# Kernel optimization log

Hardware: AMD Instinct MI355X
Metric: run time of the kernel (lower is better)

Reference implementation:

```python
import jax, jax.numpy as jnp
import numpy as np

B, D, H = 65536, 128, 64


def setup_inputs() -> dict:
    key = jax.random.key(0)
    ks = jax.random.split(key, 20)
    p = lambda k, shp, fan: jax.random.normal(k, shp, jnp.float32) * (1.0 / np.sqrt(fan))
    return {
        "l": jax.random.normal(ks[0], (B, D), jnp.float32),
        "a": jax.random.normal(ks[1], (B, D), jnp.float32),
        "v": jax.random.normal(ks[2], (B, D), jnp.float32),
        "att_w": p(ks[3], (D, 1), D), "att_b": jnp.zeros((1,), jnp.float32),
        "gf_w1": p(ks[4], (2 * D, H), 2 * D), "gf_b1": jnp.zeros((H,), jnp.float32),
        "gf_w2": p(ks[5], (H, D), H), "gf_b2": jnp.zeros((D,), jnp.float32),
        "gf2_w1": p(ks[6], (2 * D, H), 2 * D), "gf2_b1": jnp.zeros((H,), jnp.float32),
        "gf2_w2": p(ks[7], (H, D), H), "gf2_b2": jnp.zeros((D,), jnp.float32),
        "ll_w1": p(ks[8], (3 * D, H), 3 * D), "ll_b1": jnp.zeros((H,), jnp.float32),
        "ll_w2": p(ks[9], (H, H), H), "ll_b2": jnp.zeros((H,), jnp.float32),
        "ll_w3": p(ks[10], (H, D), H), "ll_b3": jnp.zeros((D,), jnp.float32),
    }


def reference(l, a, v, att_w, att_b, gf_w1, gf_b1, gf_w2, gf_b2,
              gf2_w1, gf2_b1, gf2_w2, gf2_b2,
              ll_w1, ll_b1, ll_w2, ll_b2, ll_w3, ll_b3):
    def gf(x, y):  # graph_fusion on cat([x,y],1): Linear->LeakyReLU(0.2)->Linear->Tanh
        h = jnp.concatenate([x, y], 1) @ gf_w1 + gf_b1
        h = jax.nn.leaky_relu(h, 0.2)
        return jnp.tanh(h @ gf_w2 + gf_b2)

    def gf2(x, y):
        h = jnp.concatenate([x, y], 1) @ gf2_w1 + gf2_b1
        h = jax.nn.leaky_relu(h, 0.2)
        return jnp.tanh(h @ gf2_w2 + gf2_b2)

    dot = lambda x, y: jnp.sum(x * y, axis=1)  # batched [B,1,d]@[B,d,1] -> [B]

    sa = jnp.tanh(a @ att_w + att_b)  # [B,1]
    sv = jnp.tanh(v @ att_w + att_b)
    sl = jnp.tanh(l @ att_w + att_b)

    unimodal = (sa * a + sv * v + sl * l) / 3.0  # [B,D]
    sa1, sv1, sl1 = sa[:, 0], sv[:, 0], sl[:, 0]

    # modalities are overwritten by softmax in the original
    a = jax.nn.softmax(a, axis=1)
    v = jax.nn.softmax(v, axis=1)
    l = jax.nn.softmax(l, axis=1)

    sav = (sa1 + sv1) / (dot(a, v) + 0.5)
    sal = (sa1 + sl1) / (dot(a, l) + 0.5)
    svl = (sl1 + sv1) / (dot(v, l) + 0.5)
    normalize = jax.nn.softmax(jnp.stack([sav, sal, svl], axis=1), axis=1)  # [B,3]

    gav, gal, gvl = gf(a, v), gf(a, l), gf(v, l)  # reused (torch computes twice)
    a_v = jnp.tanh(normalize[:, 0:1] * gav)
    a_l = jnp.tanh(normalize[:, 1:2] * gal)
    v_l = jnp.tanh(normalize[:, 2:3] * gvl)
    bimodal = a_v + a_l + v_l

    a_v2 = jax.nn.softmax(gav, axis=1)
    a_l2 = jax.nn.softmax(gal, axis=1)
    v_l2 = jax.nn.softmax(gvl, axis=1)

    savvl = (sav + svl) / (dot(a_v2, v_l2) + 0.5)
    saavl = (sav + sal) / (dot(a_v2, a_l2) + 0.5)
    savll = (sal + svl) / (dot(a_l2, v_l2) + 0.5)
    savl = (sav + sl1) / (dot(a_v2, l) + 0.5)
    salv = (sal + sv1) / (dot(a_l2, v) + 0.5)
    svla = (sa1 + svl) / (dot(v_l2, a) + 0.5)
    n2 = jax.nn.softmax(jnp.stack([savvl, saavl, savll, savl, salv, svla], axis=1), axis=1)

    trimodal = (jnp.tanh(n2[:, 0:1] * gf2(a_v, v_l))
                + jnp.tanh(n2[:, 1:2] * gf2(a_v, a_l))
                + jnp.tanh(n2[:, 2:3] * gf2(v_l, a_l))
                + jnp.tanh(n2[:, 3:4] * gf2(a_v, l))
                + jnp.tanh(n2[:, 4:5] * gf2(a_l, v))
                + jnp.tanh(n2[:, 5:6] * gf2(v_l, a)))

    fusion = jnp.concatenate([unimodal, bimodal, trimodal], axis=1)  # [B,3D]
    h = jnp.tanh(fusion @ ll_w1 + ll_b1)
    h = jnp.tanh(h @ ll_w2 + ll_b2)
    return jnp.tanh(h @ ll_w3 + ll_b3)
```

## Files before the change

### kernel.cpp

```cpp
#include <hip/hip_runtime.h>

typedef short bfrag __attribute__((ext_vector_type(8)));
typedef float facc  __attribute__((ext_vector_type(4)));
typedef unsigned short u16;
typedef unsigned int   u32;

#define LOG2E 1.4426950408889634f
#define MFMA(A,B,C) __builtin_amdgcn_mfma_f32_16x16x32_bf16((A),(B),(C),0,0,0)

#define AS_E 0
#define VS_E 2176
#define LS_E 4352
#define AV_E 6528
#define AL_E 8704
#define VL_E 10880
#define FUS_E 13056
#define HH_E 19328
#define SCR_B 52480
#define SM_BYTES 53504

__device__ __forceinline__ float ex2(float x){ return __builtin_amdgcn_exp2f(x); }
__device__ __forceinline__ float rcpf_(float x){ return __builtin_amdgcn_rcpf(x); }
__device__ __forceinline__ float ftanh(float x){ return 1.0f - 2.0f*rcpf_(ex2(x*(2.0f*LOG2E)) + 1.0f); }
__device__ __forceinline__ u16 f2b(float x){ return (u16)((__float_as_uint(x) + 0x8000u)>>16); }
__device__ __forceinline__ float b2f(u16 b){ return __uint_as_float(((u32)b)<<16); }
__device__ __forceinline__ u32 pk2(float x0, float x1){
  return __builtin_amdgcn_perm(__float_as_uint(x1)+0x8000u, __float_as_uint(x0)+0x8000u, 0x07060302u);
}
__device__ __forceinline__ float rsum16(float v){
  v += __shfl_xor(v,1); v += __shfl_xor(v,2); v += __shfl_xor(v,4); v += __shfl_xor(v,8); return v;
}
__device__ __forceinline__ float rmax16(float v){
  v = fmaxf(v,__shfl_xor(v,1)); v = fmaxf(v,__shfl_xor(v,2));
  v = fmaxf(v,__shfl_xor(v,4)); v = fmaxf(v,__shfl_xor(v,8)); return v;
}
__device__ __forceinline__ void st4b(u16* p, float x0,float x1,float x2,float x3){
  *(uint2*)p = make_uint2(pk2(x0,x1), pk2(x2,x3));
}

__global__ void prep_weights(const float* __restrict__ gf_w1, const float* __restrict__ gf_w2,
                             const float* __restrict__ gf2_w1, const float* __restrict__ gf2_w2,
                             const float* __restrict__ ll_w1, const float* __restrict__ ll_w2,
                             const float* __restrict__ ll_w3, u16* __restrict__ blob)
{
  u32 i = blockIdx.x*256u + threadIdx.x;
  if (i >= 86016u) return;
  u32 off, K, N; const float* src;
  if      (i < 16384u){ off=0u;     K=256u; N=64u;  src=gf_w1; }
  else if (i < 24576u){ off=16384u; K=64u;  N=128u; src=gf_w2; }
  else if (i < 40960u){ off=24576u; K=256u; N=64u;  src=gf2_w1; }
  else if (i < 49152u){ off=40960u; K=64u;  N=128u; src=gf2_w2; }
  else if (i < 73728u){ off=49152u; K=384u; N=64u;  src=ll_w1; }
  else if (i < 77824u){ off=73728u; K=64u;  N=64u;  src=ll_w2; }
  else               { off=77824u; K=64u;  N=128u; src=ll_w3; }
  u32 li = i - off, n = li / K, k = li - n*K;
  blob[i] = f2b(src[k*N + n]);
}

__global__ __launch_bounds__(256,3) void fused_graph(
    const float* __restrict__ Lg, const float* __restrict__ Ag, const float* __restrict__ Vg,
    const float* __restrict__ att_w, const float* __restrict__ att_b,
    const float* __restrict__ gf_b1, const float* __restrict__ gf_b2,
    const float* __restrict__ gf2_b1, const float* __restrict__ gf2_b2,
    const float* __restrict__ ll_b1, const float* __restrict__ ll_b2, const float* __restrict__ ll_b3,
    const u16* __restrict__ wb, float* __restrict__ out)
{
  __shared__ alignas(16) char sm[SM_BYTES];
  u16* smu = (u16*)sm;
  float* scr = (float*)(sm + SCR_B);

  const int tid = threadIdx.x;
  const int lane = tid & 63;
  const int w = tid >> 6;
  const int m = lane & 15;
  const int q = lane >> 4;
  const int er = tid >> 4;
  const int ep = tid & 15;
  const int row0 = blockIdx.x << 4;

  const int gb = (row0 + er)*128 + ep*4;
  facc A0 = *(const facc*)(Ag+gb), A1 = *(const facc*)(Ag+gb+64);
  facc V0 = *(const facc*)(Vg+gb), V1 = *(const facc*)(Vg+gb+64);
  facc L0 = *(const facc*)(Lg+gb), L1 = *(const facc*)(Lg+gb+64);
  facc W0 = *(const facc*)(att_w+ep*4), W1 = *(const facc*)(att_w+ep*4+64);
  float ab = att_b[0];
  float pa=0.f,pv=0.f,pl=0.f;
  #pragma unroll
  for (int i=0;i<4;i++){ pa += A0[i]*W0[i]+A1[i]*W1[i]; pv += V0[i]*W0[i]+V1[i]*W1[i]; pl += L0[i]*W0[i]+L1[i]*W1[i]; }
  float sa = ftanh(rsum16(pa)+ab), sv = ftanh(rsum16(pv)+ab), sl = ftanh(rsum16(pl)+ab);
  {
    u16* fu = smu + FUS_E + er*392 + ep*4;
    const float th = 1.0f/3.0f;
    st4b(fu,    (sa*A0[0]+sv*V0[0]+sl*L0[0])*th, (sa*A0[1]+sv*V0[1]+sl*L0[1])*th,
                (sa*A0[2]+sv*V0[2]+sl*L0[2])*th, (sa*A0[3]+sv*V0[3]+sl*L0[3])*th);
    st4b(fu+64, (sa*A1[0]+sv*V1[0]+sl*L1[0])*th, (sa*A1[1]+sv*V1[1]+sl*L1[1])*th,
                (sa*A1[2]+sv*V1[2]+sl*L1[2])*th, (sa*A1[3]+sv*V1[3]+sl*L1[3])*th);
  }
  #define SMAX(X0,X1,OFFE) { \
    float mx=-3.0e38f; \
    _Pragma("unroll") for (int i=0;i<4;i++){ mx=fmaxf(mx,fmaxf(X0[i],X1[i])); } \
    mx = rmax16(mx); float s_=0.f; \
    _Pragma("unroll") for (int i=0;i<4;i++){ X0[i]=ex2((X0[i]-mx)*LOG2E); X1[i]=ex2((X1[i]-mx)*LOG2E); s_+=X0[i]+X1[i]; } \
    s_ = rsum16(s_); float rs_ = rcpf_(s_); \
    _Pragma("unroll") for (int i=0;i<4;i++){ X0[i]*=rs_; X1[i]*=rs_; } \
    u16* dp_ = smu + (OFFE) + er*136 + ep*4; \
    st4b(dp_, X0[0],X0[1],X0[2],X0[3]); st4b(dp_+64, X1[0],X1[1],X1[2],X1[3]); }
  SMAX(A0,A1,AS_E)
  SMAX(V0,V1,VS_E)
  SMAX(L0,L1,LS_E)
  float dav=0.f,dal=0.f,dvl=0.f;
  #pragma unroll
  for (int i=0;i<4;i++){ dav += A0[i]*V0[i]+A1[i]*V1[i]; dal += A0[i]*L0[i]+A1[i]*L1[i]; dvl += V0[i]*L0[i]+V1[i]*L1[i]; }
  dav = rsum16(dav); dal = rsum16(dal); dvl = rsum16(dvl);
  float sav = (sa+sv)*rcpf_(dav+0.5f);
  float sal = (sa+sl)*rcpf_(dal+0.5f);
  float svl = (sl+sv)*rcpf_(dvl+0.5f);
  if (ep==0){
    float mx = fmaxf(sav,fmaxf(sal,svl));
    float e0 = ex2((sav-mx)*LOG2E), e1 = ex2((sal-mx)*LOG2E), e2 = ex2((svl-mx)*LOG2E);
    float rs = rcpf_(e0+e1+e2);
    scr[er*16+0]=e0*rs; scr[er*16+1]=e1*rs; scr[er*16+2]=e2*rs;
  }
  __syncthreads();

  const u16* g1t = wb;
  const u16* g2t = wb + 16384;
  bfrag B1[8];
  #pragma unroll
  for (int s=0;s<8;s++) B1[s] = *(const bfrag*)(g1t + (w*16+m)*256 + s*32 + q*8);
  bfrag B2[2][2];
  #pragma unroll
  for (int t=0;t<2;t++){
    #pragma unroll
    for (int s=0;s<2;s++) B2[t][s] = *(const bfrag*)(g2t + ((w+4*t)*16+m)*64 + s*32 + q*8);
  }
  facc acc0={0,0,0,0}, acc1={0,0,0,0}, acc2={0,0,0,0};
  #pragma unroll
  for (int s=0;s<8;s++){
    int k = s*32 + q*8, ko = k & 127; bool hi = (k >= 128);
    const u16* p0 = smu + (hi? VS_E:AS_E) + m*136 + ko;
    const u16* p1 = smu + (hi? LS_E:AS_E) + m*136 + ko;
    const u16* p2 = smu + (hi? LS_E:VS_E) + m*136 + ko;
    acc0 = MFMA(*(const bfrag*)p0, B1[s], acc0);
    acc1 = MFMA(*(const bfrag*)p1, B1[s], acc1);
    acc2 = MFMA(*(const bfrag*)p2, B1[s], acc2);
  }
  {
    float b1v = gf_b1[w*16+m];
    #pragma unroll
    for (int r=0;r<4;r++){
      int rr = q*4+r;
      float h0 = acc0[r]+b1v; h0 = fmaxf(h0, 0.2f*h0);
      float h1 = acc1[r]+b1v; h1 = fmaxf(h1, 0.2f*h1);
      float h2 = acc2[r]+b1v; h2 = fmaxf(h2, 0.2f*h2);
      smu[HH_E + 0*1152 + rr*72 + w*16+m] = f2b(h0);
      smu[HH_E + 1*1152 + rr*72 + w*16+m] = f2b(h1);
      smu[HH_E + 2*1152 + rr*72 + w*16+m] = f2b(h2);
    }
  }
  __syncthreads();
  facc c2[3][2] = {{{0,0,0,0},{0,0,0,0}},{{0,0,0,0},{0,0,0,0}},{{0,0,0,0},{0,0,0,0}}};
  #pragma unroll
  for (int s=0;s<2;s++){
    int k = s*32 + q*8;
    #pragma unroll
    for (int p3=0;p3<3;p3++){
      bfrag Af = *(const bfrag*)(smu + HH_E + p3*1152 + m*72 + k);
      c2[p3][0] = MFMA(Af, B2[0][s], c2[p3][0]);
      c2[p3][1] = MFMA(Af, B2[1][s], c2[p3][1]);
    }
  }
  __syncthreads();
  {
    float b2v0 = gf_b2[w*16+m], b2v1 = gf_b2[(w+4)*16+m];
    float bim[2][4] = {{0,0,0,0},{0,0,0,0}};
    float nv[4][3];
    #pragma unroll
    for (int r=0;r<4;r++){ int rr=q*4+r; nv[r][0]=scr[rr*16+0]; nv[r][1]=scr[rr*16+1]; nv[r][2]=scr[rr*16+2]; }
    #pragma unroll
    for (int p3=0;p3<3;p3++){
      #pragma unroll
      for (int t=0;t<2;t++){
        float bb = t? b2v1 : b2v0;
        int cc = (w+4*t)*16+m;
        #pragma unroll
        for (int r=0;r<4;r++){
          int rr=q*4+r;
          float g = ftanh(c2[p3][t][r] + bb);
          smu[HH_E + p3*2048 + rr*128 + cc] = f2b(g);
          float tt = ftanh(nv[r][p3]*g);
          smu[AV_E + p3*2176 + rr*136 + cc] = f2b(tt);
          bim[t][r] += tt;
        }
      }
    }
    #pragma unroll
    for (int t=0;t<2;t++){
      #pragma unroll
      for (int r=0;r<4;r++)
        smu[FUS_E + (q*4+r)*392 + 128 + (w+4*t)*16+m] = f2b(bim[t][r]);
    }
  }
  __syncthreads();

  float E0[8], E1[8], E2[8];
  #define GSTAT(EA, G3) { \
    const u16* gp_ = smu + HH_E + (G3)*2048 + er*128 + ep*4; \
    float x_[8]; \
    _Pragma("unroll") for (int i=0;i<4;i++){ x_[i]=b2f(gp_[i]); x_[4+i]=b2f(gp_[64+i]); } \
    float mx_=-3.0e38f; \
    _Pragma("unroll") for (int j=0;j<8;j++) mx_=fmaxf(mx_,x_[j]); \
    mx_ = rmax16(mx_); float s_=0.f; \
    _Pragma("unroll") for (int j=0;j<8;j++){ x_[j]=ex2((x_[j]-mx_)*LOG2E); s_+=x_[j]; } \
    s_ = rsum16(s_); float rs_=rcpf_(s_); \
    _Pragma("unroll") for (int j=0;j<8;j++) EA[j]=x_[j]*rs_; }
  GSTAT(E0,0)
  GSTAT(E1,1)
  GSTAT(E2,2)
  float d01=0.f,d02=0.f,d12=0.f,d0l=0.f,d1v=0.f,d2a=0.f;
  #pragma unroll
  for (int i=0;i<4;i++){
    d01 += E0[i]*E1[i] + E0[4+i]*E1[4+i];
    d02 += E0[i]*E2[i] + E0[4+i]*E2[4+i];
    d12 += E1[i]*E2[i] + E1[4+i]*E2[4+i];
    d0l += E0[i]*L0[i] + E0[4+i]*L1[i];
    d1v += E1[i]*V0[i] + E1[4+i]*V1[i];
    d2a += E2[i]*A0[i] + E2[4+i]*A1[i];
  }
  d01=rsum16(d01); d02=rsum16(d02); d12=rsum16(d12);
  d0l=rsum16(d0l); d1v=rsum16(d1v); d2a=rsum16(d2a);
  if (ep==0){
    float x0 = (sav+svl)*rcpf_(d02+0.5f);
    float x1 = (sav+sal)*rcpf_(d01+0.5f);
    float x2 = (sal+svl)*rcpf_(d12+0.5f);
    float x3 = (sav+sl )*rcpf_(d0l+0.5f);
    float x4 = (sal+sv )*rcpf_(d1v+0.5f);
    float x5 = (sa +svl)*rcpf_(d2a+0.5f);
    float mx = fmaxf(fmaxf(fmaxf(x0,x1),fmaxf(x2,x3)),fmaxf(x4,x5));
    float e0=ex2((x0-mx)*LOG2E), e1=ex2((x1-mx)*LOG2E), e2=ex2((x2-mx)*LOG2E);
    float e3=ex2((x3-mx)*LOG2E), e4=ex2((x4-mx)*LOG2E), e5=ex2((x5-mx)*LOG2E);
    float rs = rcpf_(e0+e1+e2+e3+e4+e5);
    scr[er*16+ 9]=e0*rs; scr[er*16+10]=e1*rs; scr[er*16+11]=e2*rs;
    scr[er*16+12]=e3*rs; scr[er*16+13]=e4*rs; scr[er*16+14]=e5*rs;
  }
  __syncthreads();

  const u16* h1t = wb + 24576;
  const u16* h2t = wb + 40960;
  bfrag C1[8];
  #pragma unroll
  for (int s=0;s<8;s++) C1[s] = *(const bfrag*)(h1t + (w*16+m)*256 + s*32 + q*8);
  bfrag C2[2][2];
  #pragma unroll
  for (int t=0;t<2;t++){
    #pragma unroll
    for (int s=0;s<2;s++) C2[t][s] = *(const bfrag*)(h2t + ((w+4*t)*16+m)*64 + s*32 + q*8);
  }
  const int S0[6] = {AV_E, AV_E, VL_E, AV_E, AL_E, VL_E};
  const int S1[6] = {VL_E, AL_E, AL_E, LS_E, VS_E, AS_E};
  facc cc1[6];
  #pragma unroll
  for (int pr=0;pr<6;pr++){ facc z = {0,0,0,0}; cc1[pr] = z; }
  #pragma unroll
  for (int s=0;s<8;s++){
    int k = s*32+q*8, ko = k&127; bool hi = (k>=128);
    #pragma unroll
    for (int pr=0;pr<6;pr++){
      const u16* sp = smu + (hi? S1[pr]:S0[pr]) + m*136 + ko;
      cc1[pr] = MFMA(*(const bfrag*)sp, C1[s], cc1[pr]);
    }
  }
  {
    float b1v = gf2_b1[w*16+m];
    #pragma unroll
    for (int pr=0;pr<6;pr++){
      #pragma unroll
      for (int r=0;r<4;r++){
        float h = cc1[pr][r]+b1v; h = fmaxf(h,0.2f*h);
        smu[HH_E + pr*1152 + (q*4+r)*72 + w*16+m] = f2b(h);
      }
    }
  }
  __syncthreads();
  facc cc2[6][2];
  #pragma unroll
  for (int pr=0;pr<6;pr++){ facc z = {0,0,0,0}; cc2[pr][0]=z; cc2[pr][1]=z; }
  #pragma unroll
  for (int s=0;s<2;s++){
    int k=s*32+q*8;
    #pragma unroll
    for (int pr=0;pr<6;pr++){
      bfrag Af = *(const bfrag*)(smu + HH_E + pr*1152 + m*72 + k);
      cc2[pr][0] = MFMA(Af, C2[0][s], cc2[pr][0]);
      cc2[pr][1] = MFMA(Af, C2[1][s], cc2[pr][1]);
    }
  }
  {
    float b2v0 = gf2_b2[w*16+m], b2v1 = gf2_b2[(w+4)*16+m];
    float tri[2][4] = {{0,0,0,0},{0,0,0,0}};
    float n2v[4][6];
    #pragma unroll
    for (int r=0;r<4;r++){
      #pragma unroll
      for (int j=0;j<6;j++) n2v[r][j] = scr[(q*4+r)*16+9+j];
    }
    #pragma unroll
    for (int pr=0;pr<6;pr++){
      #pragma unroll
      for (int t=0;t<2;t++){
        float bb = t? b2v1 : b2v0;
        #pragma unroll
        for (int r=0;r<4;r++){
          float g = ftanh(cc2[pr][t][r] + bb);
          tri[t][r] += ftanh(n2v[r][pr]*g);
        }
      }
    }
    #pragma unroll
    for (int t=0;t<2;t++){
      #pragma unroll
      for (int r=0;r<4;r++)
        smu[FUS_E + (q*4+r)*392 + 256 + (w+4*t)*16+m] = f2b(tri[t][r]);
    }
  }
  __syncthreads();

  const u16* lw1 = wb + 49152;
  const u16* lw2 = wb + 73728;
  const u16* lw3 = wb + 77824;
  {
    facc c = {0,0,0,0};
    #pragma unroll
    for (int s=0;s<12;s++){
      bfrag Bf = *(const bfrag*)(lw1 + (w*16+m)*384 + s*32 + q*8);
      bfrag Af = *(const bfrag*)(smu + FUS_E + m*392 + s*32 + q*8);
      c = MFMA(Af, Bf, c);
    }
    float b = ll_b1[w*16+m];
    #pragma unroll
    for (int r=0;r<4;r++) smu[HH_E + (q*4+r)*72 + w*16+m] = f2b(ftanh(c[r]+b));
  }
  __syncthreads();
  {
    facc c = {0,0,0,0};
    #pragma unroll
    for (int s=0;s<2;s++){
      bfrag Bf = *(const bfrag*)(lw2 + (w*16+m)*64 + s*32 + q*8);
      bfrag Af = *(const bfrag*)(smu + HH_E + m*72 + s*32 + q*8);
      c = MFMA(Af, Bf, c);
    }
    float b = ll_b2[w*16+m];
    #pragma unroll
    for (int r=0;r<4;r++) smu[HH_E + 1152 + (q*4+r)*72 + w*16+m] = f2b(ftanh(c[r]+b));
  }
  __syncthreads();
  {
    facc c0={0,0,0,0}, c1={0,0,0,0};
    #pragma unroll
    for (int s=0;s<2;s++){
      bfrag Af  = *(const bfrag*)(smu + HH_E + 1152 + m*72 + s*32 + q*8);
      bfrag Bf0 = *(const bfrag*)(lw3 + (w*16+m)*64 + s*32 + q*8);
      bfrag Bf1 = *(const bfrag*)(lw3 + ((w+4)*16+m)*64 + s*32 + q*8);
      c0 = MFMA(Af, Bf0, c0);
      c1 = MFMA(Af, Bf1, c1);
    }
    float b0 = ll_b3[w*16+m], b1 = ll_b3[(w+4)*16+m];
    #pragma unroll
    for (int r=0;r<4;r++){
      out[(row0+q*4+r)*128 + w*16+m]        = ftanh(c0[r]+b0);
      out[(row0+q*4+r)*128 + (w+4)*16+m]    = ftanh(c1[r]+b1);
    }
  }
}

extern "C" void kernel_launch(void* const* d_in, const int* in_sizes, int n_in,
                              void* d_out, int out_size, void* d_ws, size_t ws_size,
                              hipStream_t stream)
{
  const float* l      = (const float*)d_in[0];
  const float* a      = (const float*)d_in[1];
  const float* v      = (const float*)d_in[2];
  const float* att_w  = (const float*)d_in[3];
  const float* att_b  = (const float*)d_in[4];
  const float* gf_w1  = (const float*)d_in[5];
  const float* gf_b1  = (const float*)d_in[6];
  const float* gf_w2  = (const float*)d_in[7];
  const float* gf_b2  = (const float*)d_in[8];
  const float* gf2_w1 = (const float*)d_in[9];
  const float* gf2_b1 = (const float*)d_in[10];
  const float* gf2_w2 = (const float*)d_in[11];
  const float* gf2_b2 = (const float*)d_in[12];
  const float* ll_w1  = (const float*)d_in[13];
  const float* ll_b1  = (const float*)d_in[14];
  const float* ll_w2  = (const float*)d_in[15];
  const float* ll_b2  = (const float*)d_in[16];
  const float* ll_w3  = (const float*)d_in[17];
  const float* ll_b3  = (const float*)d_in[18];
  u16* blob = (u16*)d_ws;

  prep_weights<<<336, 256, 0, stream>>>(gf_w1, gf_w2, gf2_w1, gf2_w2, ll_w1, ll_w2, ll_w3, blob);
  fused_graph<<<4096, 256, 0, stream>>>(l, a, v, att_w, att_b,
                                        gf_b1, gf_b2, gf2_b1, gf2_b2,
                                        ll_b1, ll_b2, ll_b3, blob, (float*)d_out);
}
```

Before: 255.5 us.

## Shrink shared memory by reusing softmax buffers for fusion, raise occupancy, use DPP reductions

```diff
diff --git a/kernel.cpp b/kernel.cpp
--- a/kernel.cpp
+++ b/kernel.cpp
@@ -14,10 +14,9 @@
 #define AV_E 6528
 #define AL_E 8704
 #define VL_E 10880
-#define FUS_E 13056
-#define HH_E 19328
-#define SCR_B 52480
-#define SM_BYTES 53504
+#define HH_E 13056
+#define SCR_B 39936
+#define SM_BYTES 40704
 
 __device__ __forceinline__ float ex2(float x){ return __builtin_amdgcn_exp2f(x); }
 __device__ __forceinline__ float rcpf_(float x){ return __builtin_amdgcn_rcpf(x); }
@@ -27,12 +26,16 @@
 __device__ __forceinline__ u32 pk2(float x0, float x1){
   return __builtin_amdgcn_perm(__float_as_uint(x1)+0x8000u, __float_as_uint(x0)+0x8000u, 0x07060302u);
 }
+template<int N>
+__device__ __forceinline__ float ror16f(float v){
+  return __int_as_float(__builtin_amdgcn_update_dpp(0, __float_as_int(v), 0x120|N, 0xF, 0xF, false));
+}
 __device__ __forceinline__ float rsum16(float v){
-  v += __shfl_xor(v,1); v += __shfl_xor(v,2); v += __shfl_xor(v,4); v += __shfl_xor(v,8); return v;
+  v += ror16f<8>(v); v += ror16f<4>(v); v += ror16f<2>(v); v += ror16f<1>(v); return v;
 }
 __device__ __forceinline__ float rmax16(float v){
-  v = fmaxf(v,__shfl_xor(v,1)); v = fmaxf(v,__shfl_xor(v,2));
-  v = fmaxf(v,__shfl_xor(v,4)); v = fmaxf(v,__shfl_xor(v,8)); return v;
+  v = fmaxf(v,ror16f<8>(v)); v = fmaxf(v,ror16f<4>(v));
+  v = fmaxf(v,ror16f<2>(v)); v = fmaxf(v,ror16f<1>(v)); return v;
 }
 __device__ __forceinline__ void st4b(u16* p, float x0,float x1,float x2,float x3){
   *(uint2*)p = make_uint2(pk2(x0,x1), pk2(x2,x3));
@@ -57,7 +60,7 @@
   blob[i] = f2b(src[k*N + n]);
 }
 
-__global__ __launch_bounds__(256,3) void fused_graph(
+__global__ __launch_bounds__(256,4) void fused_graph(
     const float* __restrict__ Lg, const float* __restrict__ Ag, const float* __restrict__ Vg,
     const float* __restrict__ att_w, const float* __restrict__ att_b,
     const float* __restrict__ gf_b1, const float* __restrict__ gf_b2,
@@ -88,13 +91,13 @@
   #pragma unroll
   for (int i=0;i<4;i++){ pa += A0[i]*W0[i]+A1[i]*W1[i]; pv += V0[i]*W0[i]+V1[i]*W1[i]; pl += L0[i]*W0[i]+L1[i]*W1[i]; }
   float sa = ftanh(rsum16(pa)+ab), sv = ftanh(rsum16(pv)+ab), sl = ftanh(rsum16(pl)+ab);
-  {
-    u16* fu = smu + FUS_E + er*392 + ep*4;
+  u32 uni_pk[4];
+  {
     const float th = 1.0f/3.0f;
-    st4b(fu,    (sa*A0[0]+sv*V0[0]+sl*L0[0])*th, (sa*A0[1]+sv*V0[1]+sl*L0[1])*th,
-                (sa*A0[2]+sv*V0[2]+sl*L0[2])*th, (sa*A0[3]+sv*V0[3]+sl*L0[3])*th);
-    st4b(fu+64, (sa*A1[0]+sv*V1[0]+sl*L1[0])*th, (sa*A1[1]+sv*V1[1]+sl*L1[1])*th,
-                (sa*A1[2]+sv*V1[2]+sl*L1[2])*th, (sa*A1[3]+sv*V1[3]+sl*L1[3])*th);
+    uni_pk[0] = pk2((sa*A0[0]+sv*V0[0]+sl*L0[0])*th, (sa*A0[1]+sv*V0[1]+sl*L0[1])*th);
+    uni_pk[1] = pk2((sa*A0[2]+sv*V0[2]+sl*L0[2])*th, (sa*A0[3]+sv*V0[3]+sl*L0[3])*th);
+    uni_pk[2] = pk2((sa*A1[0]+sv*V1[0]+sl*L1[0])*th, (sa*A1[1]+sv*V1[1]+sl*L1[1])*th);
+    uni_pk[3] = pk2((sa*A1[2]+sv*V1[2]+sl*L1[2])*th, (sa*A1[3]+sv*V1[3]+sl*L1[3])*th);
   }
   #define SMAX(X0,X1,OFFE) { \
     float mx=-3.0e38f; \
@@ -119,7 +122,7 @@
     float mx = fmaxf(sav,fmaxf(sal,svl));
     float e0 = ex2((sav-mx)*LOG2E), e1 = ex2((sal-mx)*LOG2E), e2 = ex2((svl-mx)*LOG2E);
     float rs = rcpf_(e0+e1+e2);
-    scr[er*16+0]=e0*rs; scr[er*16+1]=e1*rs; scr[er*16+2]=e2*rs;
+    scr[er*12+0]=e0*rs; scr[er*12+1]=e1*rs; scr[er*12+2]=e2*rs;
   }
   __syncthreads();
 
@@ -171,12 +174,12 @@
     }
   }
   __syncthreads();
+  float bim[2][4] = {{0,0,0,0},{0,0,0,0}};
   {
     float b2v0 = gf_b2[w*16+m], b2v1 = gf_b2[(w+4)*16+m];
-    float bim[2][4] = {{0,0,0,0},{0,0,0,0}};
     float nv[4][3];
     #pragma unroll
-    for (int r=0;r<4;r++){ int rr=q*4+r; nv[r][0]=scr[rr*16+0]; nv[r][1]=scr[rr*16+1]; nv[r][2]=scr[rr*16+2]; }
+    for (int r=0;r<4;r++){ int rr=q*4+r; nv[r][0]=scr[rr*12+0]; nv[r][1]=scr[rr*12+1]; nv[r][2]=scr[rr*12+2]; }
     #pragma unroll
     for (int p3=0;p3<3;p3++){
       #pragma unroll
@@ -187,27 +190,23 @@
         for (int r=0;r<4;r++){
           int rr=q*4+r;
           float g = ftanh(c2[p3][t][r] + bb);
-          smu[HH_E + p3*2048 + rr*128 + cc] = f2b(g);
+          smu[HH_E + p3*2176 + rr*136 + cc] = f2b(g);
           float tt = ftanh(nv[r][p3]*g);
           smu[AV_E + p3*2176 + rr*136 + cc] = f2b(tt);
           bim[t][r] += tt;
         }
       }
     }
-    #pragma unroll
-    for (int t=0;t<2;t++){
-      #pragma unroll
-      for (int r=0;r<4;r++)
-        smu[FUS_E + (q*4+r)*392 + 128 + (w+4*t)*16+m] = f2b(bim[t][r]);
-    }
   }
   __syncthreads();
 
   float E0[8], E1[8], E2[8];
   #define GSTAT(EA, G3) { \
-    const u16* gp_ = smu + HH_E + (G3)*2048 + er*128 + ep*4; \
+    const u16* gp_ = smu + HH_E + (G3)*2176 + er*136 + ep*4; \
+    ushort4 ga_ = *(const ushort4*)gp_; ushort4 gb_ = *(const ushort4*)(gp_+64); \
     float x_[8]; \
-    _Pragma("unroll") for (int i=0;i<4;i++){ x_[i]=b2f(gp_[i]); x_[4+i]=b2f(gp_[64+i]); } \
+    x_[0]=b2f(ga_.x); x_[1]=b2f(ga_.y); x_[2]=b2f(ga_.z); x_[3]=b2f(ga_.w); \
+    x_[4]=b2f(gb_.x); x_[5]=b2f(gb_.y); x_[6]=b2f(gb_.z); x_[7]=b2f(gb_.w); \
     float mx_=-3.0e38f; \
     _Pragma("unroll") for (int j=0;j<8;j++) mx_=fmaxf(mx_,x_[j]); \
     mx_ = rmax16(mx_); float s_=0.f; \
@@ -240,8 +239,8 @@
     float e0=ex2((x0-mx)*LOG2E), e1=ex2((x1-mx)*LOG2E), e2=ex2((x2-mx)*LOG2E);
     float e3=ex2((x3-mx)*LOG2E), e4=ex2((x4-mx)*LOG2E), e5=ex2((x5-mx)*LOG2E);
     float rs = rcpf_(e0+e1+e2+e3+e4+e5);
-    scr[er*16+ 9]=e0*rs; scr[er*16+10]=e1*rs; scr[er*16+11]=e2*rs;
-    scr[er*16+12]=e3*rs; scr[er*16+13]=e4*rs; scr[er*16+14]=e5*rs;
+    scr[er*12+3]=e0*rs; scr[er*12+4]=e1*rs; scr[er*12+5]=e2*rs;
+    scr[er*12+6]=e3*rs; scr[er*12+7]=e4*rs; scr[er*12+8]=e5*rs;
   }
   __syncthreads();
 
@@ -302,7 +301,7 @@
     #pragma unroll
     for (int r=0;r<4;r++){
       #pragma unroll
-      for (int j=0;j<6;j++) n2v[r][j] = scr[(q*4+r)*16+9+j];
+      for (int j=0;j<6;j++) n2v[r][j] = scr[(q*4+r)*12+3+j];
     }
     #pragma unroll
     for (int pr=0;pr<6;pr++){
@@ -319,9 +318,13 @@
     #pragma unroll
     for (int t=0;t<2;t++){
       #pragma unroll
-      for (int r=0;r<4;r++)
-        smu[FUS_E + (q*4+r)*392 + 256 + (w+4*t)*16+m] = f2b(tri[t][r]);
-    }
+      for (int r=0;r<4;r++){
+        smu[LS_E + (q*4+r)*136 + (w+4*t)*16+m] = f2b(tri[t][r]);
+        smu[VS_E + (q*4+r)*136 + (w+4*t)*16+m] = f2b(bim[t][r]);
+      }
+    }
+    *(uint2*)(smu + AS_E + er*136 + ep*4)      = make_uint2(uni_pk[0], uni_pk[1]);
+    *(uint2*)(smu + AS_E + er*136 + ep*4 + 64) = make_uint2(uni_pk[2], uni_pk[3]);
   }
   __syncthreads();
 
@@ -332,8 +335,9 @@
     facc c = {0,0,0,0};
     #pragma unroll
     for (int s=0;s<12;s++){
+      const int base = (s<4)? AS_E : (s<8)? VS_E : LS_E;
       bfrag Bf = *(const bfrag*)(lw1 + (w*16+m)*384 + s*32 + q*8);
-      bfrag Af = *(const bfrag*)(smu + FUS_E + m*392 + s*32 + q*8);
+      bfrag Af = *(const bfrag*)(smu + base + m*136 + (s&3)*32 + q*8);
       c = MFMA(Af, Bf, c);
     }
     float b = ll_b1[w*16+m];
```

After: 249.5 us. -2.3%, faster.
